# Performance work log

Measured on AMD Instinct MI355X. Metric: run time of the kernel, lower is better.

Reference implementation:

```python
import jax, jax.numpy as jnp
import numpy as np

# BasicLS (deep_gnss): batched weighted least squares x_hat = pinv(W A) (W r)
# with W = diag(ones) == identity, so WA == A and Wr == r mathematically.
# A = [-los_x, -los_y, -los_z, 1] per measurement, r = pseudorange residual.

B = 262144  # batch of GNSS epochs
M = 32      # satellite measurements per epoch
DIM = 4     # [residual, los_x, los_y, los_z]


def setup_inputs() -> dict:
    key = jax.random.key(0)
    kx, _ = jax.random.split(key)
    x = jax.random.normal(kx, (B, M, DIM), dtype=jnp.float32)
    pad_mask = jnp.zeros((B, M), dtype=bool)  # unused by the module's forward
    return {"x": x, "pad_mask": pad_mask}


def reference(x, pad_mask):
    Bb, Mm, _ = x.shape
    # A: [B, M, 4] = concat(-x[:,:,1:4], ones)
    A = jnp.concatenate([-x[:, :, 1:4], jnp.ones((Bb, Mm, 1), dtype=x.dtype)], axis=-1)
    r = x[:, :, 0:1]  # [B, M, 1]
    # W = diag_embed(ones) is the identity, so WA = A and Wr = r.
    A_pinv = jnp.linalg.pinv(A)          # [B, 4, M] (SVD-based, matches torch.pinverse)
    out = jnp.matmul(A_pinv, r)[..., 0]  # [B, 4]
    return out
```

## Files before the change

kernel.cpp:

```cpp
#include <hip/hip_runtime.h>


#define GLOBAL_AS __attribute__((address_space(1)))
#define LDS_AS    __attribute__((address_space(3)))

__device__ __forceinline__ void async_copy16(const float4* gptr, float4* lptr) {
    __builtin_amdgcn_global_load_lds((const GLOBAL_AS void*)gptr,
                                     (LDS_AS void*)lptr, 16, 0, 0);
}

__global__ __launch_bounds__(64) void basicls_kernel(const float* __restrict__ x,
                                                     float* __restrict__ out) {
    __shared__ float4 tile[64 * 32];

    const int t  = threadIdx.x;
    const int b0 = blockIdx.x * 64;

    const float4* src = reinterpret_cast<const float4*>(x) + (size_t)b0 * 32;
#pragma unroll
    for (int k = 0; k < 32; ++k) {
        async_copy16(src + k * 64 + t, tile + k * 64);
    }
    __syncthreads();

    const int base = t * 32;
    float s11 = 0.f, s12 = 0.f, s13 = 0.f, s22 = 0.f, s23 = 0.f, s33 = 0.f;
    float s1 = 0.f, s2 = 0.f, s3 = 0.f;
    float t1 = 0.f, t2 = 0.f, t3 = 0.f, t0 = 0.f;

#pragma unroll
    for (int m = 0; m < 32; ++m) {
        int idx = base + ((m + t) & 31);
        float4 v = tile[idx];
        float r  = v.x;
        float a1 = v.y, a2 = v.z, a3 = v.w;
        s11 = fmaf(a1, a1, s11);
        s12 = fmaf(a1, a2, s12);
        s13 = fmaf(a1, a3, s13);
        s22 = fmaf(a2, a2, s22);
        s23 = fmaf(a2, a3, s23);
        s33 = fmaf(a3, a3, s33);
        s1 += a1; s2 += a2; s3 += a3;
        t1 = fmaf(a1, r, t1);
        t2 = fmaf(a2, r, t2);
        t3 = fmaf(a3, r, t3);
        t0 += r;
    }

    float G[4][4];
    G[0][0] = s11; G[0][1] = s12; G[0][2] = s13; G[0][3] = -s1;
    G[1][0] = s12; G[1][1] = s22; G[1][2] = s23; G[1][3] = -s2;
    G[2][0] = s13; G[2][1] = s23; G[2][2] = s33; G[2][3] = -s3;
    G[3][0] = -s1; G[3][1] = -s2; G[3][2] = -s3; G[3][3] = 32.0f;
    float rhs[4] = { -t1, -t2, -t3, t0 };

    float L[4][4];
#pragma unroll
    for (int k = 0; k < 4; ++k) {
        float d = G[k][k];
#pragma unroll
        for (int j = 0; j < 4; ++j) {
            if (j < k) d = fmaf(-L[k][j], L[k][j], d);
        }
        float lkk = sqrtf(fmaxf(d, 1e-30f));
        L[k][k] = lkk;
        float inv = __frcp_rn(lkk);
#pragma unroll
        for (int i = 0; i < 4; ++i) {
            if (i > k) {
                float s = G[i][k];
#pragma unroll
                for (int j = 0; j < 4; ++j) {
                    if (j < k) s = fmaf(-L[i][j], L[k][j], s);
                }
                L[i][k] = s * inv;
            }
        }
    }

    float y[4];
#pragma unroll
    for (int i = 0; i < 4; ++i) {
        float s = rhs[i];
#pragma unroll
        for (int j = 0; j < 4; ++j) {
            if (j < i) s = fmaf(-L[i][j], y[j], s);
        }
        y[i] = s * __frcp_rn(L[i][i]);
    }

    float w[4];
#pragma unroll
    for (int i = 3; i >= 0; --i) {
        float s = y[i];
#pragma unroll
        for (int j = 0; j < 4; ++j) {
            if (j > i) s = fmaf(-L[j][i], w[j], s);
        }
        w[i] = s * __frcp_rn(L[i][i]);
    }

    reinterpret_cast<float4*>(out)[b0 + t] = make_float4(w[0], w[1], w[2], w[3]);
}

extern "C" void kernel_launch(void* const* d_in, const int* in_sizes, int n_in,
                              void* d_out, int out_size, void* d_ws, size_t ws_size,
                              hipStream_t stream) {
    const float* x = (const float*)d_in[0];
    float* out = (float*)d_out;
    int B = in_sizes[0] / (32 * 4);
    dim3 block(64);
    dim3 grid(B / 64);
    basicls_kernel<<<grid, block, 0, stream>>>(x, out);
}
```

Baseline: 201.2 us.

## Split each batch element's reduction across four lanes with quad shuffles

Each block now uses 256 threads, so four wavefronts share the 64 epochs. Every epoch's 32 measurements are split across four lanes of eight each, and the partial sums are combined with xor shuffles. The aim is more parallelism per epoch and more waves in flight to hide memory latency, while keeping the same 32 KB LDS tile per block. The cost is that the Cholesky solve is computed redundantly on four lanes and only one of them stores the result.

```diff
diff --git a/kernel.cpp b/kernel.cpp
--- a/kernel.cpp
+++ b/kernel.cpp
@@ -9,29 +9,34 @@
                                      (LDS_AS void*)lptr, 16, 0, 0);
 }
 
-__global__ __launch_bounds__(64) void basicls_kernel(const float* __restrict__ x,
-                                                     float* __restrict__ out) {
-    __shared__ float4 tile[64 * 32];
+__global__ __launch_bounds__(256) void basicls_kernel(const float* __restrict__ x,
+                                                      float* __restrict__ out) {
+    __shared__ float4 tile[4 * 512];
 
-    const int t  = threadIdx.x;
-    const int b0 = blockIdx.x * 64;
+    const int tid = threadIdx.x;
+    const int w   = tid >> 6;
+    const int t   = tid & 63;
+    const int b0  = blockIdx.x * 64;
 
-    const float4* src = reinterpret_cast<const float4*>(x) + (size_t)b0 * 32;
+    const float4* src = reinterpret_cast<const float4*>(x) + (size_t)(b0 + w * 16) * 32;
+    float4* chunk = tile + w * 512;
 #pragma unroll
-    for (int k = 0; k < 32; ++k) {
-        async_copy16(src + k * 64 + t, tile + k * 64);
+    for (int k = 0; k < 8; ++k) {
+        async_copy16(src + k * 64 + t, chunk + k * 64);
     }
     __syncthreads();
 
-    const int base = t * 32;
+    const int g   = t >> 2;
+    const int sub = t & 3;
+
     float s11 = 0.f, s12 = 0.f, s13 = 0.f, s22 = 0.f, s23 = 0.f, s33 = 0.f;
     float s1 = 0.f, s2 = 0.f, s3 = 0.f;
     float t1 = 0.f, t2 = 0.f, t3 = 0.f, t0 = 0.f;
 
 #pragma unroll
-    for (int m = 0; m < 32; ++m) {
-        int idx = base + ((m + t) & 31);
-        float4 v = tile[idx];
+    for (int j = 0; j < 8; ++j) {
+        int jj = (j + g) & 7;
+        float4 v = chunk[g * 32 + sub * 8 + jj];
         float r  = v.x;
         float a1 = v.y, a2 = v.z, a3 = v.w;
         s11 = fmaf(a1, a1, s11);
@@ -46,6 +51,16 @@
         t3 = fmaf(a3, r, t3);
         t0 += r;
     }
+
+#define QUAD_REDUCE(v) \
+    v += __shfl_xor(v, 1); \
+    v += __shfl_xor(v, 2);
+    QUAD_REDUCE(s11) QUAD_REDUCE(s12) QUAD_REDUCE(s13)
+    QUAD_REDUCE(s22) QUAD_REDUCE(s23) QUAD_REDUCE(s33)
+    QUAD_REDUCE(s1)  QUAD_REDUCE(s2)  QUAD_REDUCE(s3)
+    QUAD_REDUCE(t1)  QUAD_REDUCE(t2)  QUAD_REDUCE(t3)
+    QUAD_REDUCE(t0)
+#undef QUAD_REDUCE
 
     float G[4][4];
     G[0][0] = s11; G[0][1] = s12; G[0][2] = s13; G[0][3] = -s1;
@@ -89,18 +104,21 @@
         y[i] = s * __frcp_rn(L[i][i]);
     }
 
-    float w[4];
+    float wv[4];
 #pragma unroll
     for (int i = 3; i >= 0; --i) {
         float s = y[i];
 #pragma unroll
         for (int j = 0; j < 4; ++j) {
-            if (j > i) s = fmaf(-L[j][i], w[j], s);
+            if (j > i) s = fmaf(-L[j][i], wv[j], s);
         }
-        w[i] = s * __frcp_rn(L[i][i]);
+        wv[i] = s * __frcp_rn(L[i][i]);
     }
 
-    reinterpret_cast<float4*>(out)[b0 + t] = make_float4(w[0], w[1], w[2], w[3]);
+    if (sub == 0) {
+        int b = b0 + w * 16 + g;
+        reinterpret_cast<float4*>(out)[b] = make_float4(wv[0], wv[1], wv[2], wv[3]);
+    }
 }
 
 extern "C" void kernel_launch(void* const* d_in, const int* in_sizes, int n_in,
@@ -109,7 +127,7 @@
     const float* x = (const float*)d_in[0];
     float* out = (float*)d_out;
     int B = in_sizes[0] / (32 * 4);
-    dim3 block(64);
+    dim3 block(256);
     dim3 grid(B / 64);
     basicls_kernel<<<grid, block, 0, stream>>>(x, out);
 }
```

New measurement: 199.0 us. Within noise of the previous version (-1.1%).
